# Kernel optimization log

Measured on AMD Instinct MI355X. Metric: run time of the kernel, lower is better.

Reference implementation:

```python
import jax, jax.numpy as jnp
import numpy as np
from jax import lax

RADIUS = 0.1
K = 32
STRIDE = 4
BN_EPS = 1e-5


def fps(xyz, m):
    """Furthest point sampling. xyz: (B,N,3) -> idx (B,m) int32. Starts at index 0."""
    B, N, _ = xyz.shape

    def body(carry, _):
        dists, last_idx = carry  # (B,N), (B,)
        last = jnp.take_along_axis(xyz, last_idx[:, None, None], axis=1)  # (B,1,3)
        d = jnp.sum((xyz - last) ** 2, axis=-1)  # (B,N)
        dists = jnp.minimum(dists, d)
        nxt = jnp.argmax(dists, axis=1).astype(jnp.int32)
        return (dists, nxt), nxt

    init_idx = jnp.zeros((B,), jnp.int32)
    init_d = jnp.full((B, N), 1e10, xyz.dtype)
    _, idxs = lax.scan(body, (init_d, init_idx), None, length=m - 1)  # (m-1,B)
    return jnp.concatenate([init_idx[None, :], idxs], axis=0).T  # (B,m)


def ball_query(new_xyz, xyz, radius, k):
    """First-k-in-index-order points within radius (pointnet2 semantics).
    new_xyz: (B,M,3), xyz: (B,N,3) -> idx (B,M,k). Slots past the count are
    filled with the first valid index."""
    B, N, _ = xyz.shape
    d2 = jnp.sum((new_xyz[:, :, None, :] - xyz[:, None, :, :]) ** 2, axis=-1)  # (B,M,N)
    mask = d2 < radius * radius
    order = jnp.where(mask, jnp.arange(N, dtype=jnp.int32), N)
    first_k = jnp.sort(order, axis=-1)[..., :k]  # (B,M,k)
    valid = first_k < N
    first = first_k[..., :1]  # centroid itself is always within radius
    return jnp.where(valid, first_k, first)


def setup_inputs() -> dict:
    key = jax.random.key(0)
    ks = jax.random.split(key, 8)
    B, N, C0, C1, C2 = 2, 8192, 64, 128, 256
    xyz = jax.random.uniform(ks[0], (B, N, 3), jnp.float32)
    x = jax.random.normal(ks[1], (B, C0, N), jnp.float32)
    W1 = jax.random.normal(ks[2], (C1, 3 + C0), jnp.float32) * 0.05
    b1 = jnp.zeros((C1,), jnp.float32)
    W2 = jax.random.normal(ks[3], (C2, C1), jnp.float32) * 0.05
    b2 = jnp.zeros((C2,), jnp.float32)
    gamma = jnp.ones((C2,), jnp.float32)
    beta = jnp.zeros((C2,), jnp.float32)
    return dict(xyz=xyz, x=x, W1=W1, b1=b1, W2=W2, b2=b2, gamma=gamma, beta=beta)


def reference(xyz, x, W1, b1, W2, b2, gamma, beta):
    B, N, _ = xyz.shape
    M = N // STRIDE
    fidx = fps(xyz, M)                                   # (B,M)
    b = jnp.arange(B)[:, None]
    new_xyz = xyz[b, fidx]                               # (B,M,3)
    idx = ball_query(new_xyz, xyz, RADIUS, K)            # (B,M,K)
    bi = jnp.arange(B)[:, None, None]
    rel = xyz[bi, idx] - new_xyz[:, :, None, :]          # (B,M,K,3) relative coords
    feats = jnp.transpose(x, (0, 2, 1))                  # (B,N,C0)
    group = jnp.concatenate([rel, feats[bi, idx]], axis=-1)  # (B,M,K,3+C0), xyz first
    # pointwise MLP (1x1 convs)
    h = jax.nn.relu(jnp.einsum('bmkc,oc->bmko', group, W1) + b1)
    h = jnp.einsum('bmkc,oc->bmko', h, W2) + b2          # (B,M,K,C2)
    p = jnp.max(h, axis=2)                               # (B,M,C2) max-pool over neighbors
    # BatchNorm1d, training-mode batch stats (biased variance)
    mean = jnp.mean(p, axis=(0, 1))
    var = jnp.var(p, axis=(0, 1))
    out = (p - mean) / jnp.sqrt(var + BN_EPS) * gamma + beta
    return new_xyz, jnp.transpose(out, (0, 2, 1))        # (B,M,3), (B,C2,M)
```

## Files before the change

kernel.cpp:

```cpp
#include <hip/hip_runtime.h>
#include <cstdint>
#include <cstddef>

#define B_   2
#define N_   8192
#define M_   2048
#define K_   32
#define C0_  64
#define C1_  128
#define C2_  256
#define CIN_ 67

__device__ __forceinline__ float sqdist_rn(float ax, float ay, float az,
                                           float bx, float by, float bz) {
  float dx = __fsub_rn(ax, bx);
  float dy = __fsub_rn(ay, by);
  float dz = __fsub_rn(az, bz);
  return __fadd_rn(__fadd_rn(__fmul_rn(dx, dx), __fmul_rn(dy, dy)),
                   __fmul_rn(dz, dz));
}

__device__ __forceinline__ int morton8(int ix, int iy, int iz) {
  int m = 0;
#pragma unroll
  for (int b = 0; b < 3; ++b) {
    m |= (((ix >> b) & 1) << (3 * b + 2)) | (((iy >> b) & 1) << (3 * b + 1)) |
         (((iz >> b) & 1) << (3 * b + 0));
  }
  return m;
}

__device__ __forceinline__ float wave_max_f32_dpp(float v) {
  int x = __float_as_int(v);
#define FPS_STEP(ctrl)                                                      \
  {                                                                         \
    int y = __builtin_amdgcn_update_dpp(x, x, ctrl, 0xf, 0xf, false);       \
    x = __float_as_int(fmaxf(__int_as_float(x), __int_as_float(y)));        \
  }
  FPS_STEP(0x111)
  FPS_STEP(0x112)
  FPS_STEP(0x114)
  FPS_STEP(0x118)
  FPS_STEP(0x142)
  FPS_STEP(0x143)
#undef FPS_STEP
  return __int_as_float(__builtin_amdgcn_readlane(x, 63));
}

__global__ __launch_bounds__(1024, 1) void fps_kernel(const float* __restrict__ xyz,
                                                      float* __restrict__ new_xyz) {
  const int b = blockIdx.x;
  const int t = threadIdx.x;
  const int lane = t & 63;
  const int w = t >> 6;
  const float* xb = xyz + (size_t)b * N_ * 3;

  __shared__ float sx[N_], sy[N_], sz[N_];
  __shared__ int sid[N_];
  __shared__ int hist[512];
  __shared__ int boff[512];
  __shared__ int wsum[8];
  __shared__ unsigned long long sKey[16];
  __shared__ int sPos[16];
  __shared__ float snew[M_ * 3];

  if (t < 512) hist[t] = 0;
  __syncthreads();
#pragma unroll
  for (int rr = 0; rr < 8; ++rr) {
    int i = rr * 1024 + t;
    float X = xb[i * 3 + 0], Y = xb[i * 3 + 1], Z = xb[i * 3 + 2];
    int ix = min(7, max(0, (int)(X * 8.0f)));
    int iy = min(7, max(0, (int)(Y * 8.0f)));
    int iz = min(7, max(0, (int)(Z * 8.0f)));
    atomicAdd(&hist[morton8(ix, iy, iz)], 1);
  }
  __syncthreads();
  {
    int ov = (t < 512) ? hist[t] : 0;
    int v = ov;
#pragma unroll
    for (int off = 1; off < 64; off <<= 1) {
      int n = __shfl_up(v, off);
      if (lane >= off) v += n;
    }
    if (t < 512 && lane == 63) wsum[w] = v;
    __syncthreads();
    if (t == 0) {
      int acc = 0;
#pragma unroll
      for (int j = 0; j < 8; ++j) { int x0 = wsum[j]; wsum[j] = acc; acc += x0; }
    }
    __syncthreads();
    if (t < 512) boff[t] = v - ov + wsum[w];
  }
  __syncthreads();
#pragma unroll
  for (int rr = 0; rr < 8; ++rr) {
    int i = rr * 1024 + t;
    float X = xb[i * 3 + 0], Y = xb[i * 3 + 1], Z = xb[i * 3 + 2];
    int ix = min(7, max(0, (int)(X * 8.0f)));
    int iy = min(7, max(0, (int)(Y * 8.0f)));
    int iz = min(7, max(0, (int)(Z * 8.0f)));
    int pos = atomicAdd(&boff[morton8(ix, iy, iz)], 1);
    sx[pos] = X; sy[pos] = Y; sz[pos] = Z; sid[pos] = i;
  }

  if (t == 0) {
    snew[0] = xb[0]; snew[1] = xb[1]; snew[2] = xb[2];
  }
  __syncthreads();

  float px[8], py[8], pz[8], d[8];
  int pid[8];
#pragma unroll
  for (int k = 0; k < 8; ++k) {
    int p = 8 * t + k;
    px[k] = sx[p]; py[k] = sy[p]; pz[k] = sz[p]; pid[k] = sid[p];
    d[k] = 1e10f;
  }
  float cx = 0.f, cy = 0.f, cz = 0.f;
#pragma unroll
  for (int k = 0; k < 8; ++k) { cx += px[k]; cy += py[k]; cz += pz[k]; }
  cx *= 0.125f; cy *= 0.125f; cz *= 0.125f;
  float r2m = 0.f;
#pragma unroll
  for (int k = 0; k < 8; ++k) {
    float dx = px[k] - cx, dy = py[k] - cy, dz = pz[k] - cz;
    r2m = fmaxf(r2m, dx * dx + dy * dy + dz * dz);
  }
  const float rad = sqrtf(r2m) * 1.00002f + 1e-12f;

  float bd = 1e10f;
  int bpid = pid[0], bpos = 8 * t;

  for (int it = 1; it < M_; ++it) {
    const float lx = snew[(it - 1) * 3 + 0];
    const float ly = snew[(it - 1) * 3 + 1];
    const float lz = snew[(it - 1) * 3 + 2];

    float ex = lx - cx, ey = ly - cy, ez = lz - cz;
    float dc2 = ex * ex + ey * ey + ez * ez;
    float s = sqrtf(dc2) - rad;
    bool skip = (s > 0.f) && (s * s > bd * 1.0001f);
    if (!skip) {
      float nbd = -1.f; int nbi = 0, nbp = 0;
#pragma unroll
      for (int k = 0; k < 8; ++k) {
        float dist = sqdist_rn(px[k], py[k], pz[k], lx, ly, lz);
        float dm = fminf(d[k], dist);
        d[k] = dm;
        bool take = (dm > nbd) || (dm == nbd && pid[k] < nbi);
        nbd = take ? dm : nbd;
        nbi = take ? pid[k] : nbi;
        nbp = take ? (8 * t + k) : nbp;
      }
      bd = nbd; bpid = nbi; bpos = nbp;
    }
    unsigned long long dirty = __ballot(!skip);
    if (dirty != 0ull) {
      float wmax = wave_max_f32_dpp(bd);
      unsigned long long tied = __ballot(bd == wmax);
      int bestpid = 0x7FFFFFFF, wl = 0;
      while (tied) {
        int l = __ffsll(tied) - 1;
        tied &= tied - 1;
        int p = __builtin_amdgcn_readlane(bpid, l);
        if (p < bestpid) { bestpid = p; wl = l; }
      }
      int wpos = __builtin_amdgcn_readlane(bpos, wl);
      if (lane == 0) {
        sKey[w] = ((unsigned long long)(unsigned)__float_as_int(wmax) << 32) |
                  (unsigned)(0xFFFFFFFFu - (unsigned)bestpid);
        sPos[w] = wpos;
      }
    }
    __syncthreads();
    if (w == 0) {
      int sl = lane & 15;
      unsigned long long key = sKey[sl];
      int pos = sPos[sl];
#define FPS_STEP2(ctrl)                                                        \
      {                                                                        \
        int klo = (int)(unsigned)key, khi = (int)(unsigned)(key >> 32);        \
        int olo = __builtin_amdgcn_update_dpp(klo, klo, ctrl, 0xf, 0xf, false);\
        int ohi = __builtin_amdgcn_update_dpp(khi, khi, ctrl, 0xf, 0xf, false);\
        int ops = __builtin_amdgcn_update_dpp(pos, pos, ctrl, 0xf, 0xf, false);\
        unsigned long long okey =                                              \
            ((unsigned long long)(unsigned)ohi << 32) | (unsigned)olo;         \
        if (okey > key) { key = okey; pos = ops; }                             \
      }
      FPS_STEP2(0x111)
      FPS_STEP2(0x112)
      FPS_STEP2(0x114)
      FPS_STEP2(0x118)
#undef FPS_STEP2
      int winPos = __builtin_amdgcn_readlane(pos, 15);
      float wx = sx[winPos], wy = sy[winPos], wz = sz[winPos];
      if (lane == 0) {
        snew[it * 3 + 0] = wx;
        snew[it * 3 + 1] = wy;
        snew[it * 3 + 2] = wz;
      }
    }
    __syncthreads();
  }

  for (int i = t; i < M_ * 3; i += 1024) {
    new_xyz[(size_t)b * M_ * 3 + i] = snew[i];
  }
}

__global__ __launch_bounds__(256) void mlp_kernel(const float* __restrict__ xyz,
                                                  const float* __restrict__ x,
                                                  const float* __restrict__ W1,
                                                  const float* __restrict__ b1,
                                                  const float* __restrict__ W2,
                                                  const float* __restrict__ b2,
                                                  const float* __restrict__ new_xyz,
                                                  float* __restrict__ outp) {
  __shared__ float sGRed[32 * 69];
  __shared__ float sU[128 * 69];
  __shared__ float sH1[32 * 132];
  __shared__ int sWIdx[4][K_];
  __shared__ int sWCnt[4];
  __shared__ int sIdx[K_];
  __shared__ float sQ[3];

  const int gm = blockIdx.x;
  const int b = gm >> 11;
  const int m = gm & 2047;
  const int t = threadIdx.x;
  const int lane = t & 63;
  const int w = t >> 6;
  const float* xb = xyz + (size_t)b * N_ * 3;

  if (t < 3) sQ[t] = new_xyz[(size_t)gm * 3 + t];
  __syncthreads();
  const float qx = sQ[0], qy = sQ[1], qz = sQ[2];
  const float R2 = (float)(0.1 * 0.1);

  {
    int cnt = 0;
    const int cbeg = w * 2048, cend = cbeg + 2048;
    for (int base = cbeg; base < cend; base += 64) {
      int p = base + lane;
      float d2 = sqdist_rn(qx, qy, qz, xb[p * 3 + 0], xb[p * 3 + 1], xb[p * 3 + 2]);
      bool valid = d2 < R2;
      unsigned long long mask = __ballot(valid);
      if (valid) {
        int pos = cnt + __popcll(mask & ((1ull << lane) - 1ull));
        if (pos < K_) sWIdx[w][pos] = p;
      }
      cnt += __popcll(mask);
      if (cnt >= K_) break;
    }
    if (lane == 0) sWCnt[w] = (cnt < K_) ? cnt : K_;
  }
  __syncthreads();
  if (t < K_) {
    int c0 = sWCnt[0], c1 = sWCnt[1], c2 = sWCnt[2], c3 = sWCnt[3];
    int s1 = c0 + c1, s2 = s1 + c2, s3 = s2 + c3;
    int j = t, idx;
    if (j < c0) idx = sWIdx[0][j];
    else if (j < s1) idx = sWIdx[1][j - c0];
    else if (j < s2) idx = sWIdx[2][j - s1];
    else if (j < s3) idx = sWIdx[3][j - s2];
    else {
      int fw = c0 ? 0 : (c1 ? 1 : (c2 ? 2 : 3));
      idx = (s3 > 0) ? sWIdx[fw][0] : 0;
    }
    sIdx[j] = idx;
  }
  __syncthreads();

  if (t < K_) {
    int id = sIdx[t];
    sGRed[t * 69 + 0] = xb[id * 3 + 0] - qx;
    sGRed[t * 69 + 1] = xb[id * 3 + 1] - qy;
    sGRed[t * 69 + 2] = xb[id * 3 + 2] - qz;
  }
  {
    int r = t & 31;
    int c0 = (t >> 5) * 8;
    int id = sIdx[r];
    const float* xf = x + ((size_t)b * C0_ + c0) * N_ + id;
#pragma unroll
    for (int j = 0; j < 8; ++j) sGRed[r * 69 + 3 + c0 + j] = xf[(size_t)j * N_];
  }
  for (int i = t; i < C1_ * CIN_; i += 256) {
    sU[(i / CIN_) * 69 + (i % CIN_)] = W1[i];
  }
  __syncthreads();

  const int ol = t & 31;
  const int rg = t >> 5;

  float acc[4][4] = {{0.f}};
  for (int c = 0; c < CIN_; ++c) {
    float g[4], wv[4];
#pragma unroll
    for (int i = 0; i < 4; ++i) g[i] = sGRed[(rg * 4 + i) * 69 + c];
#pragma unroll
    for (int j = 0; j < 4; ++j) wv[j] = sU[(ol + 32 * j) * 69 + c];
#pragma unroll
    for (int i = 0; i < 4; ++i)
#pragma unroll
      for (int j = 0; j < 4; ++j) acc[i][j] += g[i] * wv[j];
  }
#pragma unroll
  for (int j = 0; j < 4; ++j) {
    float bias = b1[ol + 32 * j];
#pragma unroll
    for (int i = 0; i < 4; ++i) {
      float v = acc[i][j] + bias;
      sH1[(rg * 4 + i) * 132 + ol + 32 * j] = fmaxf(v, 0.0f);
    }
  }

  float acc2[4][8] = {{0.f}};
  for (int ct = 0; ct < 4; ++ct) {
    __syncthreads();
    const float4* w4 = (const float4*)(W2 + (size_t)t * C1_ + ct * 32);
#pragma unroll
    for (int jj = 0; jj < 8; ++jj) {
      float4 v = w4[jj];
      sU[(jj * 4 + 0) * 256 + t] = v.x;
      sU[(jj * 4 + 1) * 256 + t] = v.y;
      sU[(jj * 4 + 2) * 256 + t] = v.z;
      sU[(jj * 4 + 3) * 256 + t] = v.w;
    }
    __syncthreads();
    for (int cc = 0; cc < 32; ++cc) {
      float h[4], wv[8];
#pragma unroll
      for (int i = 0; i < 4; ++i) h[i] = sH1[(rg * 4 + i) * 132 + ct * 32 + cc];
#pragma unroll
      for (int j = 0; j < 8; ++j) wv[j] = sU[cc * 256 + ol + 32 * j];
#pragma unroll
      for (int i = 0; i < 4; ++i)
#pragma unroll
        for (int j = 0; j < 8; ++j) acc2[i][j] += h[i] * wv[j];
    }
  }

  __syncthreads();
#pragma unroll
  for (int j = 0; j < 8; ++j) {
    float pm = acc2[0][j];
#pragma unroll
    for (int i = 1; i < 4; ++i) pm = fmaxf(pm, acc2[i][j]);
    sGRed[rg * 256 + ol + 32 * j] = pm;
  }
  __syncthreads();
  {
    int o = t;
    float v = sGRed[o];
#pragma unroll
    for (int g = 1; g < 8; ++g) v = fmaxf(v, sGRed[g * 256 + o]);
    v += b2[o];
    outp[((size_t)(b * C2_ + o)) * M_ + m] = v;
  }
}

__global__ __launch_bounds__(256) void bn_stats_kernel(const float* __restrict__ outp,
                                                       const float* __restrict__ gamma,
                                                       float* __restrict__ stats) {
  const int o = blockIdx.x;
  const int t = threadIdx.x;
  double s = 0.0, s2 = 0.0;
  for (int b = 0; b < B_; ++b) {
    const float* p = outp + ((size_t)(b * C2_ + o)) * M_;
    for (int i = t; i < M_; i += 256) {
      float v = p[i];
      s += (double)v;
      s2 += (double)v * (double)v;
    }
  }
#pragma unroll
  for (int off = 32; off > 0; off >>= 1) {
    s += __shfl_xor(s, off);
    s2 += __shfl_xor(s2, off);
  }
  __shared__ double aS[4], aS2[4];
  if ((t & 63) == 0) { aS[t >> 6] = s; aS2[t >> 6] = s2; }
  __syncthreads();
  if (t == 0) {
    double S = aS[0] + aS[1] + aS[2] + aS[3];
    double S2 = aS2[0] + aS2[1] + aS2[2] + aS2[3];
    double mean = S / (double)(B_ * M_);
    double var = S2 / (double)(B_ * M_) - mean * mean;
    float rstd = 1.0f / sqrtf((float)var + 1e-5f);
    stats[o] = (float)mean;
    stats[C2_ + o] = gamma[o] * rstd;
  }
}

__global__ __launch_bounds__(256) void bn_apply_kernel(float* __restrict__ outp,
                                                       const float* __restrict__ stats,
                                                       const float* __restrict__ beta) {
  const int i4 = blockIdx.x * 256 + threadIdx.x;
  const int ch = (i4 >> 9) & 255;
  const float mean = stats[ch];
  const float scale = stats[C2_ + ch];
  const float bt = beta[ch];
  float4 v = ((const float4*)outp)[i4];
  v.x = (v.x - mean) * scale + bt;
  v.y = (v.y - mean) * scale + bt;
  v.z = (v.z - mean) * scale + bt;
  v.w = (v.w - mean) * scale + bt;
  ((float4*)outp)[i4] = v;
}

extern "C" void kernel_launch(void* const* d_in, const int* in_sizes, int n_in,
                              void* d_out, int out_size, void* d_ws, size_t ws_size,
                              hipStream_t stream) {
  const float* xyz   = (const float*)d_in[0];
  const float* x     = (const float*)d_in[1];
  const float* W1    = (const float*)d_in[2];
  const float* b1    = (const float*)d_in[3];
  const float* W2    = (const float*)d_in[4];
  const float* b2    = (const float*)d_in[5];
  const float* gamma = (const float*)d_in[6];
  const float* beta  = (const float*)d_in[7];

  float* new_xyz = (float*)d_out;
  float* outp    = (float*)d_out + (size_t)B_ * M_ * 3;
  float* stats   = (float*)d_ws;

  fps_kernel<<<B_, 1024, 0, stream>>>(xyz, new_xyz);
  mlp_kernel<<<B_ * M_, 256, 0, stream>>>(xyz, x, W1, b1, W2, b2, new_xyz, outp);
  bn_stats_kernel<<<C2_, 256, 0, stream>>>(outp, gamma, stats);
  bn_apply_kernel<<<(B_ * C2_ * M_ / 4) / 256, 256, 0, stream>>>(outp, stats, beta);
}
```

Measured before the change: 3.320 ms.

## Cut FPS to one barrier per iteration with redundant wave reductions and packed keys

Each FPS iteration now has every wave reduce the per-wave keys redundantly, using double-buffered shared key slots. This drops the second __syncthreads and the broadcast through shared memory. Distance, point id and position are packed into a single 64-bit key, and point data is stored as float4 so one load fetches a point. Skipped threads whose cached best ties the wave max recompute their argmax locally. The risk is correctness of the packed key encoding and the tie handling.

```diff
diff --git a/kernel.cpp b/kernel.cpp
--- a/kernel.cpp
+++ b/kernel.cpp
@@ -55,13 +55,11 @@
   const int w = t >> 6;
   const float* xb = xyz + (size_t)b * N_ * 3;
 
-  __shared__ float sx[N_], sy[N_], sz[N_];
-  __shared__ int sid[N_];
+  __shared__ float4 spt[N_];
   __shared__ int hist[512];
   __shared__ int boff[512];
   __shared__ int wsum[8];
-  __shared__ unsigned long long sKey[16];
-  __shared__ int sPos[16];
+  __shared__ unsigned long long sKey[2][16];
   __shared__ float snew[M_ * 3];
 
   if (t < 512) hist[t] = 0;
@@ -103,9 +101,9 @@
     int iy = min(7, max(0, (int)(Y * 8.0f)));
     int iz = min(7, max(0, (int)(Z * 8.0f)));
     int pos = atomicAdd(&boff[morton8(ix, iy, iz)], 1);
-    sx[pos] = X; sy[pos] = Y; sz[pos] = Z; sid[pos] = i;
-  }
-
+    float4 v4; v4.x = X; v4.y = Y; v4.z = Z; v4.w = __int_as_float(i);
+    spt[pos] = v4;
+  }
   if (t == 0) {
     snew[0] = xb[0]; snew[1] = xb[1]; snew[2] = xb[2];
   }
@@ -115,8 +113,8 @@
   int pid[8];
 #pragma unroll
   for (int k = 0; k < 8; ++k) {
-    int p = 8 * t + k;
-    px[k] = sx[p]; py[k] = sy[p]; pz[k] = sz[p]; pid[k] = sid[p];
+    float4 v4 = spt[8 * t + k];
+    px[k] = v4.x; py[k] = v4.y; pz[k] = v4.z; pid[k] = __float_as_int(v4.w);
     d[k] = 1e10f;
   }
   float cx = 0.f, cy = 0.f, cz = 0.f;
@@ -132,19 +130,20 @@
   const float rad = sqrtf(r2m) * 1.00002f + 1e-12f;
 
   float bd = 1e10f;
-  int bpid = pid[0], bpos = 8 * t;
+  unsigned long long wkey = 0ull;
+
+  float lx = xb[0], ly = xb[1], lz = xb[2];
 
   for (int it = 1; it < M_; ++it) {
-    const float lx = snew[(it - 1) * 3 + 0];
-    const float ly = snew[(it - 1) * 3 + 1];
-    const float lz = snew[(it - 1) * 3 + 2];
+    const int wp = it & 1;
 
     float ex = lx - cx, ey = ly - cy, ez = lz - cz;
     float dc2 = ex * ex + ey * ey + ez * ez;
     float s = sqrtf(dc2) - rad;
     bool skip = (s > 0.f) && (s * s > bd * 1.0001f);
+    int bpid = 0, bpos = 0;
     if (!skip) {
-      float nbd = -1.f; int nbi = 0, nbp = 0;
+      float nbd = -1.f; int nbi = 0x7FFFFFFF, nbp = 0;
 #pragma unroll
       for (int k = 0; k < 8; ++k) {
         float dist = sqdist_rn(px[k], py[k], pz[k], lx, ly, lz);
@@ -160,7 +159,23 @@
     unsigned long long dirty = __ballot(!skip);
     if (dirty != 0ull) {
       float wmax = wave_max_f32_dpp(bd);
-      unsigned long long tied = __ballot(bd == wmax);
+      unsigned long long tied = __ballot(!skip ? (bd == wmax) : false);
+      unsigned long long tiedAll = __ballot(bd == wmax);
+      if (tiedAll != tied) {
+        if (skip && bd == wmax) {
+          float nbd = -1.f; int nbi = 0x7FFFFFFF, nbp = 0;
+#pragma unroll
+          for (int k = 0; k < 8; ++k) {
+            float dm = d[k];
+            bool take = (dm > nbd) || (dm == nbd && pid[k] < nbi);
+            nbd = take ? dm : nbd;
+            nbi = take ? pid[k] : nbi;
+            nbp = take ? (8 * t + k) : nbp;
+          }
+          bpid = nbi; bpos = nbp;
+        }
+        tied = tiedAll;
+      }
       int bestpid = 0x7FFFFFFF, wl = 0;
       while (tied) {
         int l = __ffsll(tied) - 1;
@@ -169,42 +184,40 @@
         if (p < bestpid) { bestpid = p; wl = l; }
       }
       int wpos = __builtin_amdgcn_readlane(bpos, wl);
-      if (lane == 0) {
-        sKey[w] = ((unsigned long long)(unsigned)__float_as_int(wmax) << 32) |
-                  (unsigned)(0xFFFFFFFFu - (unsigned)bestpid);
-        sPos[w] = wpos;
-      }
-    }
+      wkey = ((unsigned long long)(unsigned)__float_as_int(wmax) << 26) |
+             ((unsigned long long)(unsigned)(8191 - bestpid) << 13) |
+             (unsigned long long)(unsigned)wpos;
+    }
+    if (lane == 0) sKey[wp][w] = wkey;
     __syncthreads();
-    if (w == 0) {
-      int sl = lane & 15;
-      unsigned long long key = sKey[sl];
-      int pos = sPos[sl];
+
+    {
+      unsigned long long key = sKey[wp][lane & 15];
 #define FPS_STEP2(ctrl)                                                        \
       {                                                                        \
         int klo = (int)(unsigned)key, khi = (int)(unsigned)(key >> 32);        \
         int olo = __builtin_amdgcn_update_dpp(klo, klo, ctrl, 0xf, 0xf, false);\
         int ohi = __builtin_amdgcn_update_dpp(khi, khi, ctrl, 0xf, 0xf, false);\
-        int ops = __builtin_amdgcn_update_dpp(pos, pos, ctrl, 0xf, 0xf, false);\
         unsigned long long okey =                                              \
             ((unsigned long long)(unsigned)ohi << 32) | (unsigned)olo;         \
-        if (okey > key) { key = okey; pos = ops; }                             \
+        if (okey > key) key = okey;                                            \
       }
       FPS_STEP2(0x111)
       FPS_STEP2(0x112)
       FPS_STEP2(0x114)
       FPS_STEP2(0x118)
 #undef FPS_STEP2
-      int winPos = __builtin_amdgcn_readlane(pos, 15);
-      float wx = sx[winPos], wy = sy[winPos], wz = sz[winPos];
-      if (lane == 0) {
-        snew[it * 3 + 0] = wx;
-        snew[it * 3 + 1] = wy;
-        snew[it * 3 + 2] = wz;
-      }
-    }
-    __syncthreads();
-  }
+      int winPos = __builtin_amdgcn_readlane((int)(unsigned)key, 15) & 8191;
+      float4 c = spt[winPos];
+      lx = c.x; ly = c.y; lz = c.z;
+    }
+    if (t == 0) {
+      snew[it * 3 + 0] = lx;
+      snew[it * 3 + 1] = ly;
+      snew[it * 3 + 2] = lz;
+    }
+  }
+  __syncthreads();
 
   for (int i = t; i < M_ * 3; i += 1024) {
     new_xyz[(size_t)b * M_ * 3 + i] = snew[i];
```

Result: slower. 4.167 ms (+25.5%).

## Pack FPS argmax into a single 64-bit key and use float4 point storage

Applied to the files above, without the earlier changes.

Reworks the FPS inner loop so that distance, index tie-break and sorted position are packed into one 64-bit key. This lets the per-wave reduction be a plain u64 max through DPP, with no ballot/readlane loop to resolve ties and no separate position shuffle. Points are stored as float4 (xyz plus id) in shared memory, and the skip test is rewritten as a precomputed squared threshold against the centroid distance. The intent is to shorten the serial per-iteration critical path of the 2047-step loop. The cost is 64-bit DPP ops on every lane, and the bit packing assumes nonnegative distances fit in 38 bits after the shift.

```diff
diff --git a/kernel.cpp b/kernel.cpp
--- a/kernel.cpp
+++ b/kernel.cpp
@@ -30,12 +30,15 @@
   return m;
 }
 
-__device__ __forceinline__ float wave_max_f32_dpp(float v) {
-  int x = __float_as_int(v);
-#define FPS_STEP(ctrl)                                                      \
-  {                                                                         \
-    int y = __builtin_amdgcn_update_dpp(x, x, ctrl, 0xf, 0xf, false);       \
-    x = __float_as_int(fmaxf(__int_as_float(x), __int_as_float(y)));        \
+__device__ __forceinline__ unsigned long long wave_max_u64_dpp(unsigned long long k) {
+#define FPS_STEP(ctrl)                                                         \
+  {                                                                            \
+    int klo = (int)(unsigned)k, khi = (int)(unsigned)(k >> 32);                \
+    int olo = __builtin_amdgcn_update_dpp(klo, klo, ctrl, 0xf, 0xf, false);    \
+    int ohi = __builtin_amdgcn_update_dpp(khi, khi, ctrl, 0xf, 0xf, false);    \
+    unsigned long long ok =                                                    \
+        ((unsigned long long)(unsigned)ohi << 32) | (unsigned)olo;             \
+    if (ok > k) k = ok;                                                        \
   }
   FPS_STEP(0x111)
   FPS_STEP(0x112)
@@ -44,7 +47,7 @@
   FPS_STEP(0x142)
   FPS_STEP(0x143)
 #undef FPS_STEP
-  return __int_as_float(__builtin_amdgcn_readlane(x, 63));
+  return k;
 }
 
 __global__ __launch_bounds__(1024, 1) void fps_kernel(const float* __restrict__ xyz,
@@ -55,14 +58,12 @@
   const int w = t >> 6;
   const float* xb = xyz + (size_t)b * N_ * 3;
 
-  __shared__ float sx[N_], sy[N_], sz[N_];
-  __shared__ int sid[N_];
+  __shared__ float4 spt[N_];
+  __shared__ float snew3[M_ * 3];
+  __shared__ unsigned long long sKey[16];
   __shared__ int hist[512];
   __shared__ int boff[512];
   __shared__ int wsum[8];
-  __shared__ unsigned long long sKey[16];
-  __shared__ int sPos[16];
-  __shared__ float snew[M_ * 3];
 
   if (t < 512) hist[t] = 0;
   __syncthreads();
@@ -103,20 +104,22 @@
     int iy = min(7, max(0, (int)(Y * 8.0f)));
     int iz = min(7, max(0, (int)(Z * 8.0f)));
     int pos = atomicAdd(&boff[morton8(ix, iy, iz)], 1);
-    sx[pos] = X; sy[pos] = Y; sz[pos] = Z; sid[pos] = i;
-  }
-
+    float4 v4; v4.x = X; v4.y = Y; v4.z = Z; v4.w = __int_as_float(i);
+    spt[pos] = v4;
+  }
   if (t == 0) {
-    snew[0] = xb[0]; snew[1] = xb[1]; snew[2] = xb[2];
+    snew3[0] = xb[0]; snew3[1] = xb[1]; snew3[2] = xb[2];
   }
   __syncthreads();
 
   float px[8], py[8], pz[8], d[8];
-  int pid[8];
+  unsigned lowk[8];
 #pragma unroll
   for (int k = 0; k < 8; ++k) {
-    int p = 8 * t + k;
-    px[k] = sx[p]; py[k] = sy[p]; pz[k] = sz[p]; pid[k] = sid[p];
+    float4 v4 = spt[8 * t + k];
+    px[k] = v4.x; py[k] = v4.y; pz[k] = v4.z;
+    int pid = __float_as_int(v4.w);
+    lowk[k] = ((unsigned)(8191 - pid) << 13) | (unsigned)(8 * t + k);
     d[k] = 1e10f;
   }
   float cx = 0.f, cy = 0.f, cz = 0.f;
@@ -131,83 +134,67 @@
   }
   const float rad = sqrtf(r2m) * 1.00002f + 1e-12f;
 
-  float bd = 1e10f;
-  int bpid = pid[0], bpos = 8 * t;
+  unsigned long long tkey = 0ull;
+  float thrT = 3e38f;
 
   for (int it = 1; it < M_; ++it) {
-    const float lx = snew[(it - 1) * 3 + 0];
-    const float ly = snew[(it - 1) * 3 + 1];
-    const float lz = snew[(it - 1) * 3 + 2];
+    const float lx = snew3[it * 3 - 3];
+    const float ly = snew3[it * 3 - 2];
+    const float lz = snew3[it * 3 - 1];
 
     float ex = lx - cx, ey = ly - cy, ez = lz - cz;
     float dc2 = ex * ex + ey * ey + ez * ez;
-    float s = sqrtf(dc2) - rad;
-    bool skip = (s > 0.f) && (s * s > bd * 1.0001f);
-    if (!skip) {
-      float nbd = -1.f; int nbi = 0, nbp = 0;
-#pragma unroll
-      for (int k = 0; k < 8; ++k) {
-        float dist = sqdist_rn(px[k], py[k], pz[k], lx, ly, lz);
-        float dm = fminf(d[k], dist);
-        d[k] = dm;
-        bool take = (dm > nbd) || (dm == nbd && pid[k] < nbi);
-        nbd = take ? dm : nbd;
-        nbi = take ? pid[k] : nbi;
-        nbp = take ? (8 * t + k) : nbp;
+    bool dirtyLane = dc2 <= thrT;
+    if (__ballot(dirtyLane) != 0ull) {
+      if (dirtyLane) {
+        unsigned long long nk = 0ull;
+#pragma unroll
+        for (int k = 0; k < 8; ++k) {
+          float dist = sqdist_rn(px[k], py[k], pz[k], lx, ly, lz);
+          float dm = fminf(d[k], dist);
+          d[k] = dm;
+          unsigned long long key =
+              ((unsigned long long)(unsigned)__float_as_int(dm) << 26) | lowk[k];
+          nk = (key > nk) ? key : nk;
+        }
+        tkey = nk;
+        float bd = __int_as_float((int)(unsigned)(tkey >> 26));
+        float sr = sqrtf(bd * 1.0001f) + rad;
+        thrT = sr * sr;
       }
-      bd = nbd; bpid = nbi; bpos = nbp;
-    }
-    unsigned long long dirty = __ballot(!skip);
-    if (dirty != 0ull) {
-      float wmax = wave_max_f32_dpp(bd);
-      unsigned long long tied = __ballot(bd == wmax);
-      int bestpid = 0x7FFFFFFF, wl = 0;
-      while (tied) {
-        int l = __ffsll(tied) - 1;
-        tied &= tied - 1;
-        int p = __builtin_amdgcn_readlane(bpid, l);
-        if (p < bestpid) { bestpid = p; wl = l; }
-      }
-      int wpos = __builtin_amdgcn_readlane(bpos, wl);
-      if (lane == 0) {
-        sKey[w] = ((unsigned long long)(unsigned)__float_as_int(wmax) << 32) |
-                  (unsigned)(0xFFFFFFFFu - (unsigned)bestpid);
-        sPos[w] = wpos;
-      }
+      unsigned long long wk = wave_max_u64_dpp(tkey);
+      if (lane == 63) sKey[w] = wk;
     }
     __syncthreads();
     if (w == 0) {
-      int sl = lane & 15;
-      unsigned long long key = sKey[sl];
-      int pos = sPos[sl];
+      unsigned long long key = sKey[lane & 15];
 #define FPS_STEP2(ctrl)                                                        \
       {                                                                        \
         int klo = (int)(unsigned)key, khi = (int)(unsigned)(key >> 32);        \
         int olo = __builtin_amdgcn_update_dpp(klo, klo, ctrl, 0xf, 0xf, false);\
         int ohi = __builtin_amdgcn_update_dpp(khi, khi, ctrl, 0xf, 0xf, false);\
-        int ops = __builtin_amdgcn_update_dpp(pos, pos, ctrl, 0xf, 0xf, false);\
         unsigned long long okey =                                              \
             ((unsigned long long)(unsigned)ohi << 32) | (unsigned)olo;         \
-        if (okey > key) { key = okey; pos = ops; }                             \
+        if (okey > key) key = okey;                                            \
       }
       FPS_STEP2(0x111)
       FPS_STEP2(0x112)
       FPS_STEP2(0x114)
       FPS_STEP2(0x118)
 #undef FPS_STEP2
-      int winPos = __builtin_amdgcn_readlane(pos, 15);
-      float wx = sx[winPos], wy = sy[winPos], wz = sz[winPos];
+      int winPos = __builtin_amdgcn_readlane((int)(unsigned)key, 15) & 8191;
+      float4 c = spt[winPos];
       if (lane == 0) {
-        snew[it * 3 + 0] = wx;
-        snew[it * 3 + 1] = wy;
-        snew[it * 3 + 2] = wz;
+        snew3[it * 3 + 0] = c.x;
+        snew3[it * 3 + 1] = c.y;
+        snew3[it * 3 + 2] = c.z;
       }
     }
     __syncthreads();
   }
 
   for (int i = t; i < M_ * 3; i += 1024) {
-    new_xyz[(size_t)b * M_ * 3 + i] = snew[i];
+    new_xyz[(size_t)b * M_ * 3 + i] = snew3[i];
   }
 }
 
```

Measured after the change: 2.779 ms. -16.3%, faster.
